# Performance work log

Hardware: AMD Instinct MI355X
Metric: run time of the kernel (lower is better)

Reference implementation:

```python
import jax, jax.numpy as jnp
import numpy as np

B, S, D_IN, D_OUT = 8, 2048, 1024, 1024

def setup_inputs() -> dict:
    key = jax.random.key(0)
    k1, k2, k3, k4 = jax.random.split(key, 4)
    sc = 0.02
    return {
        "x": jax.random.normal(k1, (B, S, D_IN), dtype=jnp.float32),
        "Wq": jax.random.normal(k2, (D_IN, D_OUT), dtype=jnp.float32) * sc,
        "Wk": jax.random.normal(k3, (D_IN, D_OUT), dtype=jnp.float32) * sc,
        "Wv": jax.random.normal(k4, (D_IN, D_OUT), dtype=jnp.float32) * sc,
    }

def reference(x, Wq, Wk, Wv):
    b, n, _ = x.shape
    d_out = Wq.shape[1]
    q = jnp.einsum('bsd,de->bse', x, Wq)   # [b, n, d_out]
    k = jnp.einsum('bsd,de->bse', x, Wk)
    v = jnp.einsum('bsd,de->bse', x, Wv)
    scores = jnp.einsum('bie,bje->bij', q, k)  # [b, n, n]
    # causal mask: positions j > i set to -inf (triu, diagonal=1)
    causal = jnp.triu(jnp.ones((n, n), dtype=bool), k=1)
    scores = jnp.where(causal[None, :, :], -jnp.inf, scores)
    # NOTE: source applies softmax over dim=1 (query axis), scaled by sqrt(d_out)
    weights = jax.nn.softmax(scores / jnp.sqrt(jnp.float32(d_out)), axis=1)
    # dropout is identity in eval mode (p=0)
    return jnp.einsum('bij,bje->bie', weights, v)
```

## Files before the change

### kernel.cpp

```cpp
#include <hip/hip_runtime.h>
#include <hip/hip_bf16.h>


using bf16 = __hip_bfloat16;
typedef __attribute__((ext_vector_type(8))) short short8;
typedef __attribute__((ext_vector_type(4))) float f32x4;
typedef unsigned long long ull;

__device__ __forceinline__ float bfbits2f(unsigned short u) {
  return __uint_as_float((unsigned)u << 16);
}

__global__ void cvt_kernel(const float* __restrict__ in, bf16* __restrict__ out) {
  size_t i = ((size_t)blockIdx.x * 256 + threadIdx.x) * 4;
  float4 v = *(const float4*)(in + i);
  alignas(8) bf16 h[4] = {__float2bfloat16(v.x), __float2bfloat16(v.y),
                          __float2bfloat16(v.z), __float2bfloat16(v.w)};
  *(unsigned long long*)(out + i) = *(const unsigned long long*)h;
}

__global__ void wt_kernel(const float* __restrict__ W0, const float* __restrict__ W1,
                          const float* __restrict__ W2, bf16* __restrict__ Wt,
                          float* __restrict__ lbuf) {
  int tid = threadIdx.x;
  if (blockIdx.z == 3) {
    int bid = blockIdx.y * 16 + blockIdx.x;
    if (bid < 64) lbuf[bid * 256 + tid] = 0.f;
    return;
  }
  const float* W = blockIdx.z == 0 ? W0 : blockIdx.z == 1 ? W1 : W2;
  bf16* O = Wt + (size_t)blockIdx.z * 1048576ull;
  __shared__ float t[64][65];
  int n0 = blockIdx.x * 64, k0 = blockIdx.y * 64;
#pragma unroll
  for (int i = 0; i < 4; ++i) {
    int idx = i * 1024 + tid * 4;
    int r = idx >> 6, c = idx & 63;
    float4 v = *(const float4*)(W + (size_t)(k0 + r) * 1024 + n0 + c);
    t[r][c] = v.x; t[r][c + 1] = v.y; t[r][c + 2] = v.z; t[r][c + 3] = v.w;
  }
  __syncthreads();
#pragma unroll
  for (int i = 0; i < 4; ++i) {
    int idx = i * 1024 + tid * 4;
    int r = idx >> 6, c = idx & 63;
    alignas(8) bf16 h[4] = {__float2bfloat16(t[c][r]), __float2bfloat16(t[c + 1][r]),
                            __float2bfloat16(t[c + 2][r]), __float2bfloat16(t[c + 3][r])};
    *(unsigned long long*)(O + (size_t)(n0 + r) * 1024 + k0 + c) = *(const unsigned long long*)h;
  }
}

__global__ void vhat_kernel(const bf16* __restrict__ QKV, const float* __restrict__ l,
                            bf16* __restrict__ Vt) {
  int lb = blockIdx.z;
  const unsigned short* V =
      (const unsigned short*)QKV + ((size_t)lb * 3 + 2) * 2097152ull;
  bf16* O = Vt + (size_t)lb * 2097152ull;
  const float* lc = l + lb * 2048;
  __shared__ float t[64][65];
  __shared__ float rl[64];
  int j0 = blockIdx.x * 64, e0 = blockIdx.y * 64;
  int tid = threadIdx.x;
  if (tid < 64) rl[tid] = 1.0f / lc[j0 + tid];
#pragma unroll
  for (int i = 0; i < 4; ++i) {
    int idx = i * 1024 + tid * 4;
    int r = idx >> 6, c = idx & 63;
    ushort4 u = *(const ushort4*)(V + (size_t)(j0 + r) * 1024 + e0 + c);
    t[r][c] = bfbits2f(u.x); t[r][c + 1] = bfbits2f(u.y);
    t[r][c + 2] = bfbits2f(u.z); t[r][c + 3] = bfbits2f(u.w);
  }
  __syncthreads();
#pragma unroll
  for (int i = 0; i < 4; ++i) {
    int idx = i * 1024 + tid * 4;
    int r = idx >> 6, c = idx & 63;
    alignas(8) bf16 h[4] = {
        __float2bfloat16(t[c][r] * rl[c]), __float2bfloat16(t[c + 1][r] * rl[c + 1]),
        __float2bfloat16(t[c + 2][r] * rl[c + 2]), __float2bfloat16(t[c + 3][r] * rl[c + 3])};
    *(unsigned long long*)(O + (size_t)(e0 + r) * 2048 + j0 + c) = *(const unsigned long long*)h;
  }
}

template <int QA, int QB>
__device__ __forceinline__ void phase256(
    bf16 (*As)[256][64], bf16 (*Bs)[256][64], const int buf,
    f32x4 (&acc)[2][2][4][2], const int wm, const int wn, const int fm, const int kg,
    const bf16* gsrc, const int gld, bf16* ldst,
    const int srow, const int scg, const int scl, const bool vm4) {
  short8 af[2][4], bw[2][2];
#pragma unroll
  for (int i = 0; i < 4; ++i) {
    const int row = QA * 128 + wm * 64 + i * 16 + fm;
    const int x = row & 7;
#pragma unroll
    for (int ks = 0; ks < 2; ++ks)
      af[ks][i] = *(const short8*)(&As[buf][row][((ks * 4 + kg) ^ x) * 8]);
  }
#pragma unroll
  for (int j = 0; j < 2; ++j) {
    const int col = QB * 128 + wn * 32 + j * 16 + fm;
    const int x = col & 7;
#pragma unroll
    for (int ks = 0; ks < 2; ++ks)
      bw[ks][j] = *(const short8*)(&Bs[buf][col][((ks * 4 + kg) ^ x) * 8]);
  }
#pragma unroll
  for (int r = 0; r < 2; ++r)
    __builtin_amdgcn_global_load_lds(
        (const __attribute__((address_space(1))) void*)(gsrc + (size_t)(r * 64 + srow) * gld + scg),
        (__attribute__((address_space(3))) void*)(ldst + (r * 64 + srow) * 64 + scl), 16, 0, 0);
  __builtin_amdgcn_s_barrier();
  __builtin_amdgcn_s_setprio(1);
#pragma unroll
  for (int ks = 0; ks < 2; ++ks)
#pragma unroll
    for (int i = 0; i < 4; ++i)
#pragma unroll
      for (int j = 0; j < 2; ++j)
        acc[QA][QB][i][j] = __builtin_amdgcn_mfma_f32_16x16x32_bf16(
            af[ks][i], bw[ks][j], acc[QA][QB][i][j], 0, 0, 0);
  __builtin_amdgcn_s_setprio(0);
  if (vm4) {
    asm volatile("s_waitcnt vmcnt(4)" ::: "memory");
    __builtin_amdgcn_sched_barrier(0);
  }
  __builtin_amdgcn_s_barrier();
}

template <int EPI, bool VARK>
__device__ __forceinline__ void gemm256_body(
    const bf16* __restrict__ A, const bf16* __restrict__ B, void* __restrict__ Cv,
    int lda, int ldb, int ldc, int Kin, int zdivA, int zmodB,
    ull sA, ull sB, ull sC, float* __restrict__ lptr) {
  const unsigned gx = gridDim.x, gy = gridDim.y;
  const unsigned per_z = gx * gy;
  const unsigned total = per_z * gridDim.z;
  unsigned id = blockIdx.x + gx * (blockIdx.y + gy * blockIdx.z);
  unsigned lid = (id & 7) * (total >> 3) + (id >> 3);
  const unsigned bz = lid / per_z;
  unsigned rem = lid - bz * per_z;
  constexpr unsigned H = 8;
  const unsigned band = rem / (gx * H);
  const unsigned w = rem - band * (gx * H);
  const unsigned bx = w / H;
  const unsigned by_raw = band * H + (w - bx * H);
  const unsigned by = VARK ? (gy - 1 - by_raw) : by_raw;

  if constexpr (EPI == 1) {
    if (bx > by) return;
  }
  const int z = (int)bz;
  A += (ull)(z / zdivA) * sA;
  B += (ull)(z % zmodB) * sB;
  const int K = VARK ? (int)(by + 1) * 256 : Kin;
  const int NT = K >> 6, NU = NT >> 1;

  alignas(16) __shared__ bf16 As[2][256][64];
  alignas(16) __shared__ bf16 Bs[2][256][64];

  const int tid = threadIdx.x, wave = tid >> 6, lane = tid & 63;
  const int wm = wave >> 2, wn = wave & 3;
  const int fm = lane & 15, kg = lane >> 4;
  const int m0 = (int)by * 256, n0 = (int)bx * 256;
  const int srow = tid >> 3;
  const int scg = ((tid & 7) ^ (srow & 7)) * 8;
  const int scl = (tid & 7) * 8;

  const bf16* A0r = A + (size_t)m0 * lda;
  const bf16* A1r = A0r + (size_t)128 * lda;
  const bf16* B0r = B + (size_t)n0 * ldb;
  const bf16* B1r = B0r + (size_t)128 * ldb;

  f32x4 acc[2][2][4][2];
#pragma unroll
  for (int qa = 0; qa < 2; ++qa)
#pragma unroll
    for (int qb = 0; qb < 2; ++qb)
#pragma unroll
      for (int i = 0; i < 4; ++i)
#pragma unroll
        for (int j = 0; j < 2; ++j) acc[qa][qb][i][j] = (f32x4){0.f, 0.f, 0.f, 0.f};

  auto stage = [&](const bf16* g, int gld, bf16* l) {
#pragma unroll
    for (int r = 0; r < 2; ++r)
      __builtin_amdgcn_global_load_lds(
          (const __attribute__((address_space(1))) void*)(g + (size_t)(r * 64 + srow) * gld + scg),
          (__attribute__((address_space(3))) void*)(l + (r * 64 + srow) * 64 + scl), 16, 0, 0);
  };

  stage(A0r, lda, &As[0][0][0]);
  stage(B0r, ldb, &Bs[0][0][0]);
  stage(A1r, lda, &As[0][128][0]);
  stage(B1r, ldb, &Bs[0][128][0]);
  stage(A0r + 64, lda, &As[1][0][0]);
  stage(B0r + 64, ldb, &Bs[1][0][0]);
  asm volatile("s_waitcnt vmcnt(4)" ::: "memory");
  __builtin_amdgcn_sched_barrier(0);
  __builtin_amdgcn_s_barrier();

  for (int u = 0; u < NU; ++u) {
    const int t = 2 * u;
    const int k1 = (t + 1) * 64;
    const int k2 = (t + 2 < NT ? t + 2 : NT - 1) * 64;
    const int k3 = (t + 3 < NT ? t + 3 : NT - 1) * 64;
    phase256<0, 0>(As, Bs, 0, acc, wm, wn, fm, kg, A1r + k1, lda, &As[1][128][0], srow, scg, scl, false);
    phase256<0, 1>(As, Bs, 0, acc, wm, wn, fm, kg, B1r + k1, ldb, &Bs[1][128][0], srow, scg, scl, false);
    phase256<1, 0>(As, Bs, 0, acc, wm, wn, fm, kg, A0r + k2, lda, &As[0][0][0],   srow, scg, scl, false);
    phase256<1, 1>(As, Bs, 0, acc, wm, wn, fm, kg, B0r + k2, ldb, &Bs[0][0][0],   srow, scg, scl, true);
    phase256<0, 0>(As, Bs, 1, acc, wm, wn, fm, kg, A1r + k2, lda, &As[0][128][0], srow, scg, scl, false);
    phase256<0, 1>(As, Bs, 1, acc, wm, wn, fm, kg, B1r + k2, ldb, &Bs[0][128][0], srow, scg, scl, false);
    phase256<1, 0>(As, Bs, 1, acc, wm, wn, fm, kg, A0r + k3, lda, &As[1][0][0],   srow, scg, scl, false);
    phase256<1, 1>(As, Bs, 1, acc, wm, wn, fm, kg, B0r + k3, ldb, &Bs[1][0][0],   srow, scg, scl, true);
  }

  const int cr = kg * 4, cc = fm;
  if constexpr (EPI == 2) {
    float* C = (float*)Cv + (ull)z * sC;
#pragma unroll
    for (int qa = 0; qa < 2; ++qa)
#pragma unroll
      for (int qb = 0; qb < 2; ++qb)
#pragma unroll
        for (int i = 0; i < 4; ++i)
#pragma unroll
          for (int j = 0; j < 2; ++j)
#pragma unroll
            for (int r = 0; r < 4; ++r)
              C[(size_t)(m0 + qa * 128 + wm * 64 + i * 16 + cr + r) * ldc +
                (n0 + qb * 128 + wn * 32 + j * 16 + cc)] = acc[qa][qb][i][j][r];
  } else if constexpr (EPI == 0) {
    bf16* C = (bf16*)Cv + (ull)z * sC;
#pragma unroll
    for (int qa = 0; qa < 2; ++qa)
#pragma unroll
      for (int qb = 0; qb < 2; ++qb)
#pragma unroll
        for (int i = 0; i < 4; ++i)
#pragma unroll
          for (int j = 0; j < 2; ++j)
#pragma unroll
            for (int r = 0; r < 4; ++r)
              C[(size_t)(m0 + qa * 128 + wm * 64 + i * 16 + cr + r) * ldc +
                (n0 + qb * 128 + wn * 32 + j * 16 + cc)] =
                  __float2bfloat16(acc[qa][qb][i][j][r]);
  } else {
    bf16* C = (bf16*)Cv + (ull)z * sC;
    float colpart[2][2] = {{0.f, 0.f}, {0.f, 0.f}};
#pragma unroll
    for (int qa = 0; qa < 2; ++qa)
#pragma unroll
      for (int qb = 0; qb < 2; ++qb)
#pragma unroll
        for (int i = 0; i < 4; ++i)
#pragma unroll
          for (int j = 0; j < 2; ++j)
#pragma unroll
            for (int r = 0; r < 4; ++r) {
              int gm = m0 + qa * 128 + wm * 64 + i * 16 + cr + r;
              int gn = n0 + qb * 128 + wn * 32 + j * 16 + cc;
              float s = acc[qa][qb][i][j][r] * 0.03125f;
              float p = (gn <= gm) ? __expf(s) : 0.f;
              colpart[qb][j] += p;
              C[(size_t)gm * ldc + gn] = __float2bfloat16(p);
            }
    float* lbase = lptr + (size_t)z * 2048;
#pragma unroll
    for (int qb = 0; qb < 2; ++qb)
#pragma unroll
      for (int j = 0; j < 2; ++j) {
        float s = colpart[qb][j];
        s += __shfl_xor(s, 16);
        s += __shfl_xor(s, 32);
        if (lane < 16)
          atomicAdd(&lbase[n0 + qb * 128 + wn * 32 + j * 16 + lane], s);
      }
  }
}

__global__ __launch_bounds__(512, 2) void gemm_qkv(
    const bf16* __restrict__ A, const bf16* __restrict__ B, void* __restrict__ Cv,
    int lda, int ldb, int ldc, int Kin, int zdivA, int zmodB,
    ull sA, ull sB, ull sC) {
  gemm256_body<0, false>(A, B, Cv, lda, ldb, ldc, Kin, zdivA, zmodB, sA, sB, sC, nullptr);
}
__global__ __launch_bounds__(512, 2) void gemm_scores(
    const bf16* __restrict__ A, const bf16* __restrict__ B, void* __restrict__ Cv,
    int lda, int ldb, int ldc, int Kin, int zdivA, int zmodB,
    ull sA, ull sB, ull sC, float* __restrict__ lptr) {
  gemm256_body<1, false>(A, B, Cv, lda, ldb, ldc, Kin, zdivA, zmodB, sA, sB, sC, lptr);
}
__global__ __launch_bounds__(512, 2) void gemm_pv(
    const bf16* __restrict__ A, const bf16* __restrict__ B, void* __restrict__ Cv,
    int lda, int ldb, int ldc, int Kin, int zdivA, int zmodB,
    ull sA, ull sB, ull sC) {
  gemm256_body<2, true>(A, B, Cv, lda, ldb, ldc, Kin, zdivA, zmodB, sA, sB, sC, nullptr);
}

extern "C" void kernel_launch(void* const* d_in, const int* in_sizes, int n_in,
                              void* d_out, int out_size, void* d_ws, size_t ws_size,
                              hipStream_t stream) {
  const float* x = (const float*)d_in[0];
  const float* Wq = (const float*)d_in[1];
  const float* Wk = (const float*)d_in[2];
  const float* Wv = (const float*)d_in[3];
  float* out = (float*)d_out;

  constexpr unsigned long long X_EL = 2048ull * 1024;
  constexpr unsigned long long QKV_EL = 3ull * X_EL;
  constexpr unsigned long long P_EL = 2048ull * 2048;
  constexpr unsigned long long VT_EL = 1024ull * 2048;
  constexpr unsigned long long WT_B = 3ull * 1024 * 1024 * 2;
  constexpr unsigned long long LB_B = 8ull * 2048 * 4;
  constexpr unsigned long long PER_B = 2 * (X_EL + QKV_EL + P_EL + VT_EL);

  size_t NB = 1;
  for (size_t nb : {(size_t)8, (size_t)4, (size_t)2})
    if (WT_B + LB_B + nb * PER_B <= ws_size) { NB = nb; break; }

  char* p = (char*)d_ws;
  bf16* Wt = (bf16*)p;   p += WT_B;
  float* lbuf = (float*)p; p += LB_B;
  bf16* Xb = (bf16*)p;   p += 2 * NB * X_EL;
  bf16* QKV = (bf16*)p;  p += 2 * NB * QKV_EL;
  bf16* P = (bf16*)p;    p += 2 * NB * P_EL;
  bf16* Vt = (bf16*)p;

  wt_kernel<<<dim3(16, 16, 4), 256, 0, stream>>>(Wq, Wk, Wv, Wt, lbuf);

  for (size_t b0 = 0; b0 < 8; b0 += NB) {
    cvt_kernel<<<dim3((unsigned)(NB * 2048)), 256, 0, stream>>>(x + b0 * X_EL, Xb);
    gemm_qkv<<<dim3(4, 8, (unsigned)(NB * 3)), 512, 0, stream>>>(
        Xb, Wt, QKV, 1024, 1024, 1024, 1024, 3, 3, X_EL, 1048576ull, X_EL);
    gemm_scores<<<dim3(8, 8, (unsigned)NB), 512, 0, stream>>>(
        QKV, QKV + X_EL, P, 1024, 1024, 2048, 1024, 1, 1 << 30, QKV_EL, QKV_EL, P_EL,
        lbuf + b0 * 2048);
    vhat_kernel<<<dim3(32, 16, (unsigned)NB), 256, 0, stream>>>(QKV, lbuf + b0 * 2048, Vt);
    gemm_pv<<<dim3(4, 8, (unsigned)NB), 512, 0, stream>>>(
        P, Vt, out + b0 * X_EL, 2048, 2048, 1024, 0, 1, 1 << 30, P_EL, VT_EL, X_EL);
  }
}
```

Baseline: 405.0 us.

## Restructure 256x256 GEMM main loop with 128x64 wave tiles and register ping-pong

Replaces the four-quadrant phase scheme with a contiguous 128x64 tile per wave. Each wave keeps two 4x4 accumulator sets and double-buffers its A/B fragments in registers, so the LDS reads for the next MMA block are issued before the current one runs. Fewer fragment reads are needed per MFMA, which should cut LDS traffic and improve overlap. In exchange it adds full vmcnt(0)/lgkmcnt(0) drains at buffer switches and more register pressure, which may reduce occupancy at two blocks per CU.

```diff
diff --git a/kernel.cpp b/kernel.cpp
--- a/kernel.cpp
+++ b/kernel.cpp
@@ -82,51 +82,38 @@
   }
 }
 
-template <int QA, int QB>
-__device__ __forceinline__ void phase256(
-    bf16 (*As)[256][64], bf16 (*Bs)[256][64], const int buf,
-    f32x4 (&acc)[2][2][4][2], const int wm, const int wn, const int fm, const int kg,
-    const bf16* gsrc, const int gld, bf16* ldst,
-    const int srow, const int scg, const int scl, const bool vm4) {
-  short8 af[2][4], bw[2][2];
-#pragma unroll
-  for (int i = 0; i < 4; ++i) {
-    const int row = QA * 128 + wm * 64 + i * 16 + fm;
-    const int x = row & 7;
-#pragma unroll
-    for (int ks = 0; ks < 2; ++ks)
-      af[ks][i] = *(const short8*)(&As[buf][row][((ks * 4 + kg) ^ x) * 8]);
-  }
-#pragma unroll
-  for (int j = 0; j < 2; ++j) {
-    const int col = QB * 128 + wn * 32 + j * 16 + fm;
-    const int x = col & 7;
-#pragma unroll
-    for (int ks = 0; ks < 2; ++ks)
-      bw[ks][j] = *(const short8*)(&Bs[buf][col][((ks * 4 + kg) ^ x) * 8]);
-  }
-#pragma unroll
-  for (int r = 0; r < 2; ++r)
-    __builtin_amdgcn_global_load_lds(
-        (const __attribute__((address_space(1))) void*)(gsrc + (size_t)(r * 64 + srow) * gld + scg),
-        (__attribute__((address_space(3))) void*)(ldst + (r * 64 + srow) * 64 + scl), 16, 0, 0);
-  __builtin_amdgcn_s_barrier();
-  __builtin_amdgcn_s_setprio(1);
-#pragma unroll
-  for (int ks = 0; ks < 2; ++ks)
-#pragma unroll
-    for (int i = 0; i < 4; ++i)
-#pragma unroll
-      for (int j = 0; j < 2; ++j)
-        acc[QA][QB][i][j] = __builtin_amdgcn_mfma_f32_16x16x32_bf16(
-            af[ks][i], bw[ks][j], acc[QA][QB][i][j], 0, 0, 0);
-  __builtin_amdgcn_s_setprio(0);
-  if (vm4) {
-    asm volatile("s_waitcnt vmcnt(4)" ::: "memory");
-    __builtin_amdgcn_sched_barrier(0);
-  }
-  __builtin_amdgcn_s_barrier();
-}
+#define RDA(DST, BUF, QA, KS)                                                   \
+  do {                                                                          \
+    const bf16* _p = &As[BUF][0][0] + aoff + (QA)*4096;                         \
+    const int _c = (((KS)*4 + kg) ^ sw) * 8;                                    \
+    _Pragma("unroll") for (int _i = 0; _i < 4; ++_i)                            \
+        DST[_i] = *(const short8*)(_p + _i * 1024 + _c);                        \
+  } while (0)
+
+#define RDB(DST, BUF, KS)                                                       \
+  do {                                                                          \
+    const bf16* _p = &Bs[BUF][0][0] + boff;                                     \
+    const int _c = (((KS)*4 + kg) ^ sw) * 8;                                    \
+    _Pragma("unroll") for (int _j = 0; _j < 4; ++_j)                            \
+        DST[_j] = *(const short8*)(_p + _j * 1024 + _c);                        \
+  } while (0)
+
+#define MMA16(AF, BW, ACC)                                                      \
+  do {                                                                          \
+    __builtin_amdgcn_s_setprio(1);                                              \
+    _Pragma("unroll") for (int _i = 0; _i < 4; ++_i)                            \
+        _Pragma("unroll") for (int _j = 0; _j < 4; ++_j)                        \
+            ACC[_i][_j] = __builtin_amdgcn_mfma_f32_16x16x32_bf16(              \
+                AF[_i], BW[_j], ACC[_i][_j], 0, 0, 0);                          \
+    __builtin_amdgcn_s_setprio(0);                                              \
+  } while (0)
+
+#define BAR __builtin_amdgcn_s_barrier()
+#define DRAIN                                                                   \
+  do {                                                                          \
+    asm volatile("s_waitcnt vmcnt(0) lgkmcnt(0)" ::: "memory");                 \
+    __builtin_amdgcn_sched_barrier(0);                                          \
+  } while (0)
 
 template <int EPI, bool VARK>
 __device__ __forceinline__ void gemm256_body(
@@ -161,28 +148,31 @@
 
   const int tid = threadIdx.x, wave = tid >> 6, lane = tid & 63;
   const int wm = wave >> 2, wn = wave & 3;
-  const int fm = lane & 15, kg = lane >> 4;
+  const int fm = lane & 15, kg = lane >> 4, sw = fm & 7;
   const int m0 = (int)by * 256, n0 = (int)bx * 256;
   const int srow = tid >> 3;
   const int scg = ((tid & 7) ^ (srow & 7)) * 8;
   const int scl = (tid & 7) * 8;
 
+  const int aoff = (wm * 128 + fm) * 64;
+  const int boff = (wn * 64 + fm) * 64;
+
   const bf16* A0r = A + (size_t)m0 * lda;
   const bf16* A1r = A0r + (size_t)128 * lda;
   const bf16* B0r = B + (size_t)n0 * ldb;
   const bf16* B1r = B0r + (size_t)128 * ldb;
 
-  f32x4 acc[2][2][4][2];
-#pragma unroll
-  for (int qa = 0; qa < 2; ++qa)
-#pragma unroll
-    for (int qb = 0; qb < 2; ++qb)
-#pragma unroll
-      for (int i = 0; i < 4; ++i)
-#pragma unroll
-        for (int j = 0; j < 2; ++j) acc[qa][qb][i][j] = (f32x4){0.f, 0.f, 0.f, 0.f};
-
-  auto stage = [&](const bf16* g, int gld, bf16* l) {
+  f32x4 acc0[4][4], acc1[4][4];
+#pragma unroll
+  for (int i = 0; i < 4; ++i)
+#pragma unroll
+    for (int j = 0; j < 4; ++j) {
+      acc0[i][j] = (f32x4){0.f, 0.f, 0.f, 0.f};
+      acc1[i][j] = (f32x4){0.f, 0.f, 0.f, 0.f};
+    }
+  short8 afA[4], afB[4], bwA[4], bwB[4];
+
+  auto stageHalf = [&](const bf16* g, int gld, bf16* l) {
 #pragma unroll
     for (int r = 0; r < 2; ++r)
       __builtin_amdgcn_global_load_lds(
@@ -190,92 +180,107 @@
           (__attribute__((address_space(3))) void*)(l + (r * 64 + srow) * 64 + scl), 16, 0, 0);
   };
 
-  stage(A0r, lda, &As[0][0][0]);
-  stage(B0r, ldb, &Bs[0][0][0]);
-  stage(A1r, lda, &As[0][128][0]);
-  stage(B1r, ldb, &Bs[0][128][0]);
-  stage(A0r + 64, lda, &As[1][0][0]);
-  stage(B0r + 64, ldb, &Bs[1][0][0]);
+  stageHalf(A0r, lda, &As[0][0][0]);
+  stageHalf(B0r, ldb, &Bs[0][0][0]);
+  stageHalf(A1r, lda, &As[0][128][0]);
+  stageHalf(B1r, ldb, &Bs[0][128][0]);
+  stageHalf(A0r + 64, lda, &As[1][0][0]);
+  stageHalf(B0r + 64, ldb, &Bs[1][0][0]);
   asm volatile("s_waitcnt vmcnt(4)" ::: "memory");
   __builtin_amdgcn_sched_barrier(0);
-  __builtin_amdgcn_s_barrier();
+  BAR;
+  RDA(afA, 0, 0, 0);
+  RDB(bwA, 0, 0);
 
   for (int u = 0; u < NU; ++u) {
     const int t = 2 * u;
     const int k1 = (t + 1) * 64;
     const int k2 = (t + 2 < NT ? t + 2 : NT - 1) * 64;
     const int k3 = (t + 3 < NT ? t + 3 : NT - 1) * 64;
-    phase256<0, 0>(As, Bs, 0, acc, wm, wn, fm, kg, A1r + k1, lda, &As[1][128][0], srow, scg, scl, false);
-    phase256<0, 1>(As, Bs, 0, acc, wm, wn, fm, kg, B1r + k1, ldb, &Bs[1][128][0], srow, scg, scl, false);
-    phase256<1, 0>(As, Bs, 0, acc, wm, wn, fm, kg, A0r + k2, lda, &As[0][0][0],   srow, scg, scl, false);
-    phase256<1, 1>(As, Bs, 0, acc, wm, wn, fm, kg, B0r + k2, ldb, &Bs[0][0][0],   srow, scg, scl, true);
-    phase256<0, 0>(As, Bs, 1, acc, wm, wn, fm, kg, A1r + k2, lda, &As[0][128][0], srow, scg, scl, false);
-    phase256<0, 1>(As, Bs, 1, acc, wm, wn, fm, kg, B1r + k2, ldb, &Bs[0][128][0], srow, scg, scl, false);
-    phase256<1, 0>(As, Bs, 1, acc, wm, wn, fm, kg, A0r + k3, lda, &As[1][0][0],   srow, scg, scl, false);
-    phase256<1, 1>(As, Bs, 1, acc, wm, wn, fm, kg, B0r + k3, ldb, &Bs[1][0][0],   srow, scg, scl, true);
+    RDA(afB, 0, 1, 0);
+    stageHalf(A1r + k1, lda, &As[1][128][0]);
+    stageHalf(B1r + k1, ldb, &Bs[1][128][0]);
+    BAR; MMA16(afA, bwA, acc0); BAR;
+    RDA(afA, 0, 0, 1);
+    RDB(bwB, 0, 1);
+    BAR; MMA16(afB, bwA, acc1); BAR;
+    RDA(afB, 0, 1, 1);
+    BAR; MMA16(afA, bwB, acc0); DRAIN; BAR;
+    RDA(afA, 1, 0, 0);
+    RDB(bwA, 1, 0);
+    stageHalf(A0r + k2, lda, &As[0][0][0]);
+    stageHalf(B0r + k2, ldb, &Bs[0][0][0]);
+    BAR; MMA16(afB, bwB, acc1); BAR;
+    RDA(afB, 1, 1, 0);
+    stageHalf(A1r + k2, lda, &As[0][128][0]);
+    stageHalf(B1r + k2, ldb, &Bs[0][128][0]);
+    BAR; MMA16(afA, bwA, acc0); BAR;
+    RDA(afA, 1, 0, 1);
+    RDB(bwB, 1, 1);
+    BAR; MMA16(afB, bwA, acc1); BAR;
+    RDA(afB, 1, 1, 1);
+    BAR; MMA16(afA, bwB, acc0); DRAIN; BAR;
+    RDA(afA, 0, 0, 0);
+    RDB(bwA, 0, 0);
+    stageHalf(A0r + k3, lda, &As[1][0][0]);
+    stageHalf(B0r + k3, ldb, &Bs[1][0][0]);
+    BAR; MMA16(afB, bwB, acc1); BAR;
   }
 
   const int cr = kg * 4, cc = fm;
+  const int rbase = m0 + wm * 128 + cr;
+  const int cbase = n0 + wn * 64 + cc;
   if constexpr (EPI == 2) {
     float* C = (float*)Cv + (ull)z * sC;
 #pragma unroll
-    for (int qa = 0; qa < 2; ++qa)
-#pragma unroll
-      for (int qb = 0; qb < 2; ++qb)
-#pragma unroll
-        for (int i = 0; i < 4; ++i)
-#pragma unroll
-          for (int j = 0; j < 2; ++j)
-#pragma unroll
-            for (int r = 0; r < 4; ++r)
-              C[(size_t)(m0 + qa * 128 + wm * 64 + i * 16 + cr + r) * ldc +
-                (n0 + qb * 128 + wn * 32 + j * 16 + cc)] = acc[qa][qb][i][j][r];
+    for (int i = 0; i < 4; ++i)
+#pragma unroll
+      for (int j = 0; j < 4; ++j)
+#pragma unroll
+        for (int r = 0; r < 4; ++r) {
+          C[(size_t)(rbase + i * 16 + r) * ldc + (cbase + j * 16)] = acc0[i][j][r];
+          C[(size_t)(rbase + 64 + i * 16 + r) * ldc + (cbase + j * 16)] = acc1[i][j][r];
+        }
   } else if constexpr (EPI == 0) {
     bf16* C = (bf16*)Cv + (ull)z * sC;
 #pragma unroll
-    for (int qa = 0; qa < 2; ++qa)
-#pragma unroll
-      for (int qb = 0; qb < 2; ++qb)
-#pragma unroll
-        for (int i = 0; i < 4; ++i)
-#pragma unroll
-          for (int j = 0; j < 2; ++j)
-#pragma unroll
-            for (int r = 0; r < 4; ++r)
-              C[(size_t)(m0 + qa * 128 + wm * 64 + i * 16 + cr + r) * ldc +
-                (n0 + qb * 128 + wn * 32 + j * 16 + cc)] =
-                  __float2bfloat16(acc[qa][qb][i][j][r]);
+    for (int i = 0; i < 4; ++i)
+#pragma unroll
+      for (int j = 0; j < 4; ++j)
+#pragma unroll
+        for (int r = 0; r < 4; ++r) {
+          C[(size_t)(rbase + i * 16 + r) * ldc + (cbase + j * 16)] =
+              __float2bfloat16(acc0[i][j][r]);
+          C[(size_t)(rbase + 64 + i * 16 + r) * ldc + (cbase + j * 16)] =
+              __float2bfloat16(acc1[i][j][r]);
+        }
   } else {
     bf16* C = (bf16*)Cv + (ull)z * sC;
-    float colpart[2][2] = {{0.f, 0.f}, {0.f, 0.f}};
+    float colpart[4] = {0.f, 0.f, 0.f, 0.f};
 #pragma unroll
     for (int qa = 0; qa < 2; ++qa)
 #pragma unroll
-      for (int qb = 0; qb < 2; ++qb)
-#pragma unroll
-        for (int i = 0; i < 4; ++i)
-#pragma unroll
-          for (int j = 0; j < 2; ++j)
-#pragma unroll
-            for (int r = 0; r < 4; ++r) {
-              int gm = m0 + qa * 128 + wm * 64 + i * 16 + cr + r;
-              int gn = n0 + qb * 128 + wn * 32 + j * 16 + cc;
-              float s = acc[qa][qb][i][j][r] * 0.03125f;
-              float p = (gn <= gm) ? __expf(s) : 0.f;
-              colpart[qb][j] += p;
-              C[(size_t)gm * ldc + gn] = __float2bfloat16(p);
-            }
-    float* lbase = lptr + (size_t)z * 2048;
-#pragma unroll
-    for (int qb = 0; qb < 2; ++qb)
-#pragma unroll
-      for (int j = 0; j < 2; ++j) {
-        float s = colpart[qb][j];
-        s += __shfl_xor(s, 16);
-        s += __shfl_xor(s, 32);
-        if (lane < 16)
-          atomicAdd(&lbase[n0 + qb * 128 + wn * 32 + j * 16 + lane], s);
-      }
+      for (int i = 0; i < 4; ++i)
+#pragma unroll
+        for (int j = 0; j < 4; ++j)
+#pragma unroll
+          for (int r = 0; r < 4; ++r) {
+            int gm = rbase + qa * 64 + i * 16 + r;
+            int gn = cbase + j * 16;
+            float v = qa == 0 ? acc0[i][j][r] : acc1[i][j][r];
+            float s = v * 0.03125f;
+            float p = (gn <= gm) ? __expf(s) : 0.f;
+            colpart[j] += p;
+            C[(size_t)gm * ldc + gn] = __float2bfloat16(p);
+          }
+    float* lcol = lptr + (size_t)z * 2048 + n0 + wn * 64;
+#pragma unroll
+    for (int j = 0; j < 4; ++j) {
+      float s = colpart[j];
+      s += __shfl_xor(s, 16);
+      s += __shfl_xor(s, 32);
+      if (lane < 16) atomicAdd(&lcol[j * 16 + lane], s);
+    }
   }
 }
 
```

Result: faster. 390.5 us (-3.6%).
